# Performance work log

Measured on AMD Instinct MI355X. Metric: run time of the kernel, lower is better.

## Reference

```python
import jax, jax.numpy as jnp
import numpy as np

L, LM, B, D, H, DFF = 1024, 1024, 2, 512, 8, 2048
N = 16              # mamba d_state
DI = 2 * D          # mamba d_inner (expand=2)
DCONV = 4
DTR = (D + 15) // 16  # dt_rank = 32
EPS = 1e-5


def _rmsnorm(x, w):
    return x * w / jnp.sqrt(jnp.mean(x * x, -1, keepdims=True) + EPS)


def _layernorm(x, w, b):
    m = jnp.mean(x, -1, keepdims=True)
    v = jnp.mean((x - m) ** 2, -1, keepdims=True)
    return (x - m) / jnp.sqrt(v + EPS) * w + b


def _mha(q, k, v, in_w, in_b, out_w, out_b):
    # q: [Lq,B,D]; k,v: [Lk,B,D]
    Lq, Bb, Dd = q.shape
    Lk = k.shape[0]
    dh = Dd // H
    qp = (q @ in_w[:Dd].T + in_b[:Dd]).reshape(Lq, Bb, H, dh).transpose(1, 2, 0, 3)
    kp = (k @ in_w[Dd:2 * Dd].T + in_b[Dd:2 * Dd]).reshape(Lk, Bb, H, dh).transpose(1, 2, 0, 3)
    vp = (v @ in_w[2 * Dd:].T + in_b[2 * Dd:]).reshape(Lk, Bb, H, dh).transpose(1, 2, 0, 3)
    s = jnp.einsum('bhqd,bhkd->bhqk', qp, kp) * (dh ** -0.5)
    a = jax.nn.softmax(s, axis=-1)
    o = jnp.einsum('bhqk,bhkd->bhqd', a, vp).transpose(2, 0, 1, 3).reshape(Lq, Bb, Dd)
    return o @ out_w.T + out_b, jnp.mean(a, axis=1)  # attn averaged over heads


def _mamba(x, in_w, in_b, conv_w, conv_b, xproj_w, dt_w, dt_b, Alog, Dp, out_w, out_b):
    # x: [B,L,D] -> [B,L,D] selective state-space scan (mamba.py MambaBlock)
    xz = x @ in_w.T + in_b
    xm, z = xz[..., :DI], xz[..., DI:]
    # causal depthwise conv over time (pad left d_conv-1, truncate to L)
    xc = jax.lax.conv_general_dilated(
        xm.transpose(0, 2, 1), conv_w[:, None, :], (1,), [(DCONV - 1, 0)],
        feature_group_count=DI, dimension_numbers=('NCH', 'OIH', 'NCH'))
    xm = jax.nn.silu((xc + conv_b[None, :, None]).transpose(0, 2, 1))  # [B,L,DI]
    dbc = xm @ xproj_w.T
    dt, Bs, Cs = dbc[..., :DTR], dbc[..., DTR:DTR + N], dbc[..., DTR + N:]
    delta = jax.nn.softplus(dt @ dt_w.T + dt_b)           # [B,L,DI]
    A = -jnp.exp(Alog)                                    # [DI,N]
    dA = jnp.exp(delta[..., None] * A)                    # [B,L,DI,N]
    dBx = delta[..., None] * Bs[:, :, None, :] * xm[..., None]

    def step(h, ab):
        a, b = ab
        h = a * h + b
        return h, h

    _, hs = jax.lax.scan(step, jnp.zeros((x.shape[0], DI, N), x.dtype),
                         (dA.transpose(1, 0, 2, 3), dBx.transpose(1, 0, 2, 3)))
    y = jnp.einsum('blin,bln->bli', hs.transpose(1, 0, 2, 3), Cs)
    y = (y + Dp * xm) * jax.nn.silu(z)
    return y @ out_w.T + out_b


def _bimamba(x, ln1_w, ln1_b, ln2_w, ln2_b, f1_w, f1_b, f2_w, f2_b, mp):
    xn = _layernorm(x, ln1_w, ln1_b)
    mf = _mamba(xn, *mp)
    mb = jnp.flip(_mamba(jnp.flip(xn, 1), *mp), 1)
    m = _layernorm(mf + mb, ln2_w, ln2_b)
    ff = jax.nn.gelu(m @ f1_w.T + f1_b, approximate=False) @ f2_w.T + f2_b
    return ff + x


def _forward(tgt, memory,
             sa_in_w, sa_in_b, sa_out_w, sa_out_b,
             ca_in_w, ca_in_b, ca_out_w, ca_out_b,
             n1_w, n2_w, n3_w, n4_w,
             lin1_w, lin1_b, lin2_w, lin2_b,
             ln1_w, ln1_b, ln2_w, ln2_b,
             bff1_w, bff1_b, bff2_w, bff2_b,
             m_in_w, m_in_b, m_conv_w, m_conv_b, m_xproj_w,
             m_dt_w, m_dt_b, m_Alog, m_D, m_out_w, m_out_b):
    t2, _ = _mha(tgt, tgt, tgt, sa_in_w, sa_in_b, sa_out_w, sa_out_b)
    tgt = _rmsnorm(tgt + t2, n1_w)
    t2, attn = _mha(tgt, memory, memory, ca_in_w, ca_in_b, ca_out_w, ca_out_b)
    tgt = _rmsnorm(tgt + t2, n2_w)
    x = tgt.transpose(1, 0, 2)  # l b d -> b l d
    mp = (m_in_w, m_in_b, m_conv_w, m_conv_b, m_xproj_w, m_dt_w, m_dt_b, m_Alog, m_D, m_out_w, m_out_b)
    x = x + _bimamba(x, ln1_w, ln1_b, ln2_w, ln2_b, bff1_w, bff1_b, bff2_w, bff2_b, mp)
    tgt = x.transpose(1, 0, 2)
    tgt = _rmsnorm(tgt, n3_w)
    t2 = jax.nn.relu(tgt @ lin1_w.T + lin1_b) @ lin2_w.T + lin2_b
    tgt = _rmsnorm(tgt + t2, n4_w)
    return tgt, attn


def setup_inputs() -> dict:
    key = jax.random.key(0)
    ks = jax.random.split(key, 24)
    g = lambda i, shape, s=0.02: jax.random.normal(ks[i], shape, dtype=jnp.float32) * s
    inp = {
        'tgt': jax.random.normal(ks[0], (L, B, D), dtype=jnp.float32),
        'memory': jax.random.normal(ks[1], (LM, B, D), dtype=jnp.float32),
        'sa_in_w': g(2, (3 * D, D)), 'sa_in_b': jnp.zeros((3 * D,)),
        'sa_out_w': g(3, (D, D)), 'sa_out_b': jnp.zeros((D,)),
        'ca_in_w': g(4, (3 * D, D)), 'ca_in_b': jnp.zeros((3 * D,)),
        'ca_out_w': g(5, (D, D)), 'ca_out_b': jnp.zeros((D,)),
        'n1_w': jnp.ones((D,)), 'n2_w': jnp.ones((D,)),
        'n3_w': jnp.ones((D,)), 'n4_w': jnp.ones((D,)),
        'lin1_w': g(6, (DFF, D)), 'lin1_b': jnp.zeros((DFF,)),
        'lin2_w': g(7, (D, DFF)), 'lin2_b': jnp.zeros((D,)),
        'ln1_w': jnp.ones((D,)), 'ln1_b': jnp.zeros((D,)),
        'ln2_w': jnp.ones((D,)), 'ln2_b': jnp.zeros((D,)),
        'bff1_w': g(8, (4 * D, D)), 'bff1_b': jnp.zeros((4 * D,)),
        'bff2_w': g(9, (D, 4 * D)), 'bff2_b': jnp.zeros((D,)),
        'm_in_w': g(10, (2 * DI, D)), 'm_in_b': jnp.zeros((2 * DI,)),
        'm_conv_w': g(11, (DI, DCONV), 0.1), 'm_conv_b': jnp.zeros((DI,)),
        'm_xproj_w': g(12, (DTR + 2 * N, DI)),
        'm_dt_w': g(13, (DI, DTR), 0.1), 'm_dt_b': g(14, (DI,), 0.01),
        'm_Alog': jnp.log(jnp.tile(jnp.arange(1, N + 1, dtype=jnp.float32), (DI, 1))),
        'm_D': jnp.ones((DI,)),
        'm_out_w': g(15, (D, DI)), 'm_out_b': jnp.zeros((D,)),
    }
    return inp


def reference(tgt, memory,
              sa_in_w, sa_in_b, sa_out_w, sa_out_b,
              ca_in_w, ca_in_b, ca_out_w, ca_out_b,
              n1_w, n2_w, n3_w, n4_w,
              lin1_w, lin1_b, lin2_w, lin2_b,
              ln1_w, ln1_b, ln2_w, ln2_b,
              bff1_w, bff1_b, bff2_w, bff2_b,
              m_in_w, m_in_b, m_conv_w, m_conv_b, m_xproj_w,
              m_dt_w, m_dt_b, m_Alog, m_D, m_out_w, m_out_b):
    return _forward(tgt, memory,
                    sa_in_w, sa_in_b, sa_out_w, sa_out_b,
                    ca_in_w, ca_in_b, ca_out_w, ca_out_b,
                    n1_w, n2_w, n3_w, n4_w,
                    lin1_w, lin1_b, lin2_w, lin2_b,
                    ln1_w, ln1_b, ln2_w, ln2_b,
                    bff1_w, bff1_b, bff2_w, bff2_b,
                    m_in_w, m_in_b, m_conv_w, m_conv_b, m_xproj_w,
                    m_dt_w, m_dt_b, m_Alog, m_D, m_out_w, m_out_b)
```

## Files before the change

kernel.cpp:

```cpp
#include <hip/hip_runtime.h>
#include <hip/hip_bf16.h>
#include <math.h>

#define L_SEQ 1024
#define BB 2
#define DD 512
#define HH 8
#define DFFN 2048
#define NSTATE 16
#define DI 1024
#define EPSF 1e-5f

typedef __hip_bfloat16 bf16;
typedef __attribute__((ext_vector_type(8))) short short8v;
typedef __attribute__((ext_vector_type(4))) short short4v;
typedef __attribute__((ext_vector_type(4))) float float4v;

__device__ __forceinline__ float bf2f(bf16 v){ return __bfloat162float(v); }
__device__ __forceinline__ bf16 f2bf(float v){ return __float2bfloat16(v); }
__device__ __forceinline__ short f2bfs(float v){
  bf16 t = __float2bfloat16(v);
  short s; __builtin_memcpy(&s, &t, 2);
  return s;
}

__device__ __forceinline__ void powtab(float q1, float* dA){
  float q2=q1*q1, q4=q2*q2, q8=q4*q4;
  dA[0]=q1;       dA[1]=q2;       dA[2]=q2*q1;     dA[3]=q4;
  dA[4]=q4*q1;    dA[5]=q4*q2;    dA[6]=q4*q2*q1;  dA[7]=q8;
  dA[8]=q8*q1;    dA[9]=q8*q2;    dA[10]=q8*q2*q1; dA[11]=q8*q4;
  dA[12]=q8*q4*q1;dA[13]=q8*q4*q2;dA[14]=q8*q4*q2*q1;dA[15]=q8*q8;
}

__global__ void k_detect(const unsigned int* __restrict__ w, int* __restrict__ flag){
  __shared__ int cnt;
  if (threadIdx.x==0) cnt = 0;
  __syncthreads();
  unsigned int x = w[threadIdx.x];
  unsigned int low = x & 0xffffu;
  int e = (int)((low >> 7) & 0xffu);
  int vote = (low==0u) || (e >= 110 && e <= 140);
  atomicAdd(&cnt, vote);
  __syncthreads();
  if (threadIdx.x==0) flag[0] = (cnt >= 128) ? 1 : 0;
}

struct CvtTabF { const void* src[25]; unsigned int off[26]; };
struct CvtTabW { const void* src[12]; unsigned int off[13]; };

__global__ __launch_bounds__(256) void k_cvt_f32(CvtTabF t, float* __restrict__ dst,
                                                 const int* __restrict__ flag, int total){
  const int isbf = flag[0];
  for (int g = blockIdx.x*256 + threadIdx.x; g < total; g += gridDim.x*256){
    int k = 0;
    while (t.off[k+1] <= (unsigned int)g) ++k;
    int e = g - (int)t.off[k];
    dst[g] = isbf ? bf2f(((const bf16*)t.src[k])[e]) : ((const float*)t.src[k])[e];
  }
}

__global__ __launch_bounds__(256) void k_cvt_b16(CvtTabW t, bf16* __restrict__ dst,
                                                 const int* __restrict__ flag, int total){
  const int isbf = flag[0];
  for (int g = blockIdx.x*256 + threadIdx.x; g < total; g += gridDim.x*256){
    int k = 0;
    while (t.off[k+1] <= (unsigned int)g) ++k;
    int e = g - (int)t.off[k];
    if (isbf) dst[g] = ((const bf16*)t.src[k])[e];
    else      dst[g] = f2bf(((const float*)t.src[k])[e]);
  }
}

__global__ __launch_bounds__(256) void k_mfma_gemm(
    const void* __restrict__ Ab, int cA, long long sAb, long long sAh, long long sAm,
    const void* __restrict__ Bb, long long sBb, long long sBh, long long sBrow, int cB,
    void* __restrict__ Cb, int outBf, long long sCb, long long sCh, long long sCm,
    const float* __restrict__ bias, float scale, int act, int K, int H)
{
  __shared__ short As[64*40];
  __shared__ short Bs[64*40];
  const int tid = threadIdx.x;
  int bx = blockIdx.x, by = blockIdx.y;
  if (gridDim.z == 1 && (gridDim.y & 7) == 0){
    int gx = gridDim.x;
    int lin = by*gx + bx;
    int xcd = lin & 7, i = lin >> 3;
    by = xcd*(gridDim.y >> 3) + i / gx;
    bx = i % gx;
  }
  const int z = blockIdx.z; const int zb = z / H; const int zh = z % H;
  const int col0 = bx << 6, m0 = by << 6;
  const float* Af = (const float*)Ab;
  const bf16*  Aw = (const bf16*)Ab;
  const long long aoff = zb*sAb + zh*sAh;
  const float* Bf = (const float*)Bb;
  const bf16* Bw = (const bf16*)Bb;
  const long long boff = zb*sBb + zh*sBh;
  float4v acc[4];
  #pragma unroll
  for (int i=0;i<4;++i) acc[i] = (float4v)(0.f);
  const int lane = tid & 63, w = tid >> 6;
  const int lr = lane & 15, quad = lane >> 4;

  for (int k0 = 0; k0 < K; k0 += 32){
    if (cA == 1){
      int row = tid >> 2, k8 = (tid & 3) << 3;
      short8v v = *(const short8v*)&Aw[aoff + (long long)(m0+row)*sAm + k0 + k8];
      *(short8v*)&As[row*40 + k8] = v;
    } else {
      #pragma unroll
      for (int i=0;i<2;++i){
        int g = tid + i*256;
        int row = g >> 3, k4 = (g & 7) << 2;
        float4 v = *(const float4*)&Af[aoff + (long long)(m0+row)*sAm + k0 + k4];
        short4v s4; s4.x=f2bfs(v.x); s4.y=f2bfs(v.y); s4.z=f2bfs(v.z); s4.w=f2bfs(v.w);
        *(short4v*)&As[row*40 + k4] = s4;
      }
    }
    if (cB == 2){
      int row = tid >> 2, k8 = (tid & 3) << 3;
      short8v v = *(const short8v*)&Bw[boff + (long long)(col0+row)*sBrow + k0 + k8];
      *(short8v*)&Bs[row*40 + k8] = v;
    } else {
      #pragma unroll
      for (int i=0;i<2;++i){
        int g = tid + i*256;
        int row = g >> 3, k4 = (g & 7) << 2;
        float4 v = *(const float4*)&Bf[boff + (long long)(col0+row)*sBrow + k0 + k4];
        short4v s4; s4.x=f2bfs(v.x); s4.y=f2bfs(v.y); s4.z=f2bfs(v.z); s4.w=f2bfs(v.w);
        *(short4v*)&Bs[row*40 + k4] = s4;
      }
    }
    __syncthreads();
    short8v a = *(short8v*)&As[(w*16 + lr)*40 + quad*8];
    #pragma unroll
    for (int cb=0; cb<4; ++cb){
      short8v bfr = *(short8v*)&Bs[(cb*16 + lr)*40 + quad*8];
      acc[cb] = __builtin_amdgcn_mfma_f32_16x16x32_bf16(a, bfr, acc[cb], 0, 0, 0);
    }
    __syncthreads();
  }
  #pragma unroll
  for (int cb=0; cb<4; ++cb){
    #pragma unroll
    for (int r=0;r<4;++r){
      int m = m0 + w*16 + quad*4 + r;
      int n = col0 + cb*16 + lr;
      float v = acc[cb][r] * scale;
      if (bias) v += bias[n];
      if (act==1) v = fmaxf(v,0.f);
      else if (act==2) v = 0.5f*v*(1.f + erff(v*0.70710678118654752f));
      else if (act==3) v = fmaxf(v,0.f) + log1pf(__expf(-fabsf(v)));
      if (outBf) ((bf16*)Cb)[zb*sCb + zh*sCh + (long long)m*sCm + n] = f2bf(v);
      else       ((float*)Cb)[zb*sCb + zh*sCh + (long long)m*sCm + n] = v;
    }
  }
}

__global__ __launch_bounds__(256) void k_gemm_sk(
    const void* __restrict__ Ab, int cA, long long sAz, long long sAm,
    const bf16* __restrict__ Bw, long long sBrow,
    float* __restrict__ Cb, long long sCz, long long sCm,
    const float* __restrict__ bias, int K, int KS)
{
  __shared__ short As[64*40];
  __shared__ short Bs[64*40];
  const int tid = threadIdx.x;
  int bx, by, bz;
  {
    int gx = gridDim.x, gy = gridDim.y, gz = gridDim.z;
    int lin = ((int)blockIdx.z*gy + blockIdx.y)*gx + blockIdx.x;
    int xcd = lin & 7, i = lin >> 3;
    bx = i % gx; int rest = i / gx;
    int pair = xcd * ((gy*gz) >> 3) + rest;
    by = pair % gy; bz = pair / gy;
  }
  const int zb = bz / KS, kc = bz % KS;
  const int Kc = K / KS;
  const int col0 = bx << 6, m0 = by << 6;
  const float* Af = (const float*)Ab;
  const bf16*  Aw = (const bf16*)Ab;
  const long long aoff = (long long)zb*sAz;
  float4v acc[4];
  #pragma unroll
  for (int i=0;i<4;++i) acc[i] = (float4v)(0.f);
  const int lane = tid & 63, w = tid >> 6;
  const int lr = lane & 15, quad = lane >> 4;

  const int kbeg = kc*Kc;
  for (int k0 = kbeg; k0 < kbeg + Kc; k0 += 32){
    if (cA == 1){
      int row = tid >> 2, k8 = (tid & 3) << 3;
      *(short8v*)&As[row*40 + k8] =
        *(const short8v*)&Aw[aoff + (long long)(m0+row)*sAm + k0 + k8];
    } else {
      #pragma unroll
      for (int i=0;i<2;++i){
        int g = tid + i*256;
        int row = g >> 3, k4 = (g & 7) << 2;
        float4 v = *(const float4*)&Af[aoff + (long long)(m0+row)*sAm + k0 + k4];
        short4v s4; s4.x=f2bfs(v.x); s4.y=f2bfs(v.y); s4.z=f2bfs(v.z); s4.w=f2bfs(v.w);
        *(short4v*)&As[row*40 + k4] = s4;
      }
    }
    {
      int row = tid >> 2, k8 = (tid & 3) << 3;
      *(short8v*)&Bs[row*40 + k8] =
        *(const short8v*)&Bw[(long long)(col0+row)*sBrow + k0 + k8];
    }
    __syncthreads();
    short8v a = *(short8v*)&As[(w*16 + lr)*40 + quad*8];
    #pragma unroll
    for (int cb=0; cb<4; ++cb){
      short8v bfr = *(short8v*)&Bs[(cb*16 + lr)*40 + quad*8];
      acc[cb] = __builtin_amdgcn_mfma_f32_16x16x32_bf16(a, bfr, acc[cb], 0, 0, 0);
    }
    __syncthreads();
  }
  #pragma unroll
  for (int cb=0; cb<4; ++cb){
    #pragma unroll
    for (int r=0;r<4;++r){
      int m = m0 + w*16 + quad*4 + r;
      int n = col0 + cb*16 + lr;
      float v = acc[cb][r];
      if (kc == 0 && bias) v += bias[n];
      atomicAdd(&Cb[(long long)zb*sCz + (long long)m*sCm + n], v);
    }
  }
}

__global__ __launch_bounds__(256) void k_flash2(
    const bf16* __restrict__ Qb, int ldq, int qoff,
    const bf16* __restrict__ Kb, int ldk, int koff,
    const bf16* __restrict__ Vb, int ldv, int voff,
    float* __restrict__ Opart, float* __restrict__ Ml, float scale)
{
  __shared__ short Qs[64*40];
  __shared__ short Ks[64*40];
  __shared__ short Vs[64*40];
  __shared__ short Ps[64*40];
  const int tid = threadIdx.x;
  const int q0 = blockIdx.x << 6;
  const int z = blockIdx.y; const int b = z >> 3; const int hoff = (z & 7) << 6;
  const int kc = blockIdx.z;
  const int lane = tid & 63, w = tid >> 6;
  const int lr = lane & 15, quad = lane >> 4;

  #pragma unroll
  for (int i=0;i<2;++i){
    int idx = tid + i*256;
    int row = idx >> 3, d8 = (idx & 7) << 3;
    *(short8v*)&Qs[row*40 + d8] =
      *(const short8v*)&Qb[(size_t)((q0+row)*BB + b)*ldq + qoff + hoff + d8];
  }

  float m_r[4], l_r[4];
  #pragma unroll
  for (int r=0;r<4;++r){ m_r[r] = -1e30f; l_r[r] = 0.f; }
  float4v acc_o[4];
  #pragma unroll
  for (int cb=0;cb<4;++cb) acc_o[cb] = (float4v)(0.f);

  short8v kr[2], vr[2];
  #pragma unroll
  for (int i=0;i<2;++i){
    int idx = tid + i*256;
    int row = kc*128 + (idx >> 3); int d8 = (idx & 7) << 3;
    kr[i] = *(const short8v*)&Kb[(size_t)(row*BB + b)*ldk + koff + hoff + d8];
    vr[i] = *(const short8v*)&Vb[(size_t)(row*BB + b)*ldv + voff + hoff + d8];
  }

  for (int kt=0; kt<2; ++kt){
    __syncthreads();
    #pragma unroll
    for (int i=0;i<2;++i){
      int idx = tid + i*256;
      int row = idx >> 3, d8 = (idx & 7) << 3;
      *(short8v*)&Ks[row*40 + d8] = kr[i];
      int sc = row ^ d8;
      #pragma unroll
      for (int j=0;j<8;++j) Vs[(d8+j)*40 + sc] = vr[i][j];
    }
    if (kt < 1){
      #pragma unroll
      for (int i=0;i<2;++i){
        int idx = tid + i*256;
        int row = kc*128 + 64 + (idx >> 3); int d8 = (idx & 7) << 3;
        kr[i] = *(const short8v*)&Kb[(size_t)(row*BB + b)*ldk + koff + hoff + d8];
        vr[i] = *(const short8v*)&Vb[(size_t)(row*BB + b)*ldv + voff + hoff + d8];
      }
    }
    __syncthreads();
    short8v a0 = *(short8v*)&Qs[(w*16+lr)*40 + quad*8];
    short8v a1 = *(short8v*)&Qs[(w*16+lr)*40 + quad*8 + 32];
    float4v s[4];
    #pragma unroll
    for (int cb=0;cb<4;++cb){
      short8v b0 = *(short8v*)&Ks[(cb*16+lr)*40 + quad*8];
      short8v b1 = *(short8v*)&Ks[(cb*16+lr)*40 + quad*8 + 32];
      float4v t = __builtin_amdgcn_mfma_f32_16x16x32_bf16(a0, b0, (float4v)(0.f), 0,0,0);
      s[cb] = __builtin_amdgcn_mfma_f32_16x16x32_bf16(a1, b1, t, 0,0,0);
    }
    #pragma unroll
    for (int cb=0;cb<4;++cb)
      #pragma unroll
      for (int r=0;r<4;++r) s[cb][r] *= scale;
    float al[4];
    #pragma unroll
    for (int r=0;r<4;++r){
      float mx = fmaxf(fmaxf(s[0][r],s[1][r]),fmaxf(s[2][r],s[3][r]));
      #pragma unroll
      for (int ofs=1; ofs<16; ofs<<=1) mx = fmaxf(mx, __shfl_xor(mx, ofs));
      float mnew = fmaxf(m_r[r], mx);
      al[r] = __expf(m_r[r] - mnew);
      float sum = 0.f;
      #pragma unroll
      for (int cb=0;cb<4;++cb){
        float p = __expf(s[cb][r] - mnew);
        s[cb][r] = p;
        sum += p;
      }
      #pragma unroll
      for (int ofs=1; ofs<16; ofs<<=1) sum += __shfl_xor(sum, ofs);
      l_r[r] = l_r[r]*al[r] + sum;
      m_r[r] = mnew;
    }
    #pragma unroll
    for (int cb=0;cb<4;++cb)
      #pragma unroll
      for (int r=0;r<4;++r){
        acc_o[cb][r] *= al[r];
        Ps[(w*16 + quad*4 + r)*40 + cb*16 + lr] = f2bfs(s[cb][r]);
      }
    __syncthreads();
    short8v p0 = *(short8v*)&Ps[(w*16+lr)*40 + quad*8];
    short8v p1 = *(short8v*)&Ps[(w*16+lr)*40 + quad*8 + 32];
    #pragma unroll
    for (int cb=0;cb<4;++cb){
      int dcol = cb*16 + lr;
      int sw = (dcol >> 3) & 7;
      short8v v0 = *(short8v*)&Vs[dcol*40 + ((quad ^ sw) << 3)];
      short8v v1 = *(short8v*)&Vs[dcol*40 + (((quad+4) ^ sw) << 3)];
      acc_o[cb] = __builtin_amdgcn_mfma_f32_16x16x32_bf16(p0, v0, acc_o[cb], 0,0,0);
      acc_o[cb] = __builtin_amdgcn_mfma_f32_16x16x32_bf16(p1, v1, acc_o[cb], 0,0,0);
    }
  }
  #pragma unroll
  for (int r=0;r<4;++r){
    int row = q0 + w*16 + quad*4 + r;
    size_t obase = ((size_t)(kc*16 + z)*1024 + row)*64;
    #pragma unroll
    for (int cb=0;cb<4;++cb)
      Opart[obase + cb*16 + lr] = acc_o[cb][r];
    if (lr == 0){
      size_t mi = ((size_t)kc*16384 + z*1024 + row)*2;
      Ml[mi] = m_r[r]; Ml[mi+1] = l_r[r];
    }
  }
}

__global__ __launch_bounds__(256) void k_fcomb(const float* __restrict__ Opart, const float* __restrict__ Ml,
                                               bf16* __restrict__ O, float* __restrict__ Mfin)
{
  int gid = blockIdx.x*256 + threadIdx.x;
  int row = gid >> 6, d = gid & 63;
  int z = row >> 10, q = row & 1023;
  float m[8], l[8];
  #pragma unroll
  for (int kc=0;kc<8;++kc){
    size_t mi = ((size_t)kc*16384 + row)*2;
    m[kc] = Ml[mi]; l[kc] = Ml[mi+1];
  }
  float ms = -1e30f;
  #pragma unroll
  for (int kc=0;kc<8;++kc) ms = fmaxf(ms, m[kc]);
  float ls = 0.f, o = 0.f;
  #pragma unroll
  for (int kc=0;kc<8;++kc){
    float c = __expf(m[kc]-ms);
    ls += l[kc]*c;
    o  += Opart[((size_t)kc*16384 + row)*64 + d] * c;
  }
  o /= ls;
  int b = z >> 3, hoff = (z & 7) << 6;
  O[((size_t)q*BB + b)*512 + hoff + d] = f2bf(o);
  if (d == 0){ Mfin[(size_t)row*2] = ms; Mfin[(size_t)row*2+1] = ls; }
}

__global__ __launch_bounds__(256) void k_pmean(
    const bf16* __restrict__ Qb, int ldq,
    const bf16* __restrict__ Kb, int ldk,
    const float* __restrict__ Mfin, void* __restrict__ out,
    const int* __restrict__ flag, float scale)
{
  __shared__ short Qs[64*40];
  __shared__ short Ks[64*40];
  const int tid = threadIdx.x;
  const int k0 = blockIdx.x << 6, q0 = blockIdx.y << 6;
  const int b = blockIdx.z;
  const int lane = tid & 63, w = tid >> 6;
  const int lr = lane & 15, quad = lane >> 4;
  float acc[4][4];
  #pragma unroll
  for (int cb=0;cb<4;++cb)
    #pragma unroll
    for (int r=0;r<4;++r) acc[cb][r] = 0.f;

  for (int h=0; h<8; ++h){
    int z = b*8 + h, hoff = h << 6;
    __syncthreads();
    #pragma unroll
    for (int i=0;i<2;++i){
      int idx = tid + i*256;
      int row = idx >> 3, d8 = (idx & 7) << 3;
      *(short8v*)&Qs[row*40 + d8] = *(const short8v*)&Qb[((size_t)(q0+row)*BB + b)*ldq + hoff + d8];
      *(short8v*)&Ks[row*40 + d8] = *(const short8v*)&Kb[((size_t)(k0+row)*BB + b)*ldk + hoff + d8];
    }
    __syncthreads();
    float mm[4], li[4];
    #pragma unroll
    for (int r=0;r<4;++r){
      int qrow = q0 + w*16 + quad*4 + r;
      size_t mi = ((size_t)z*1024 + qrow)*2;
      mm[r] = Mfin[mi]; li[r] = 1.f/Mfin[mi+1];
    }
    short8v a0 = *(short8v*)&Qs[(w*16+lr)*40 + quad*8];
    short8v a1 = *(short8v*)&Qs[(w*16+lr)*40 + quad*8 + 32];
    #pragma unroll
    for (int cb=0;cb<4;++cb){
      short8v b0 = *(short8v*)&Ks[(cb*16+lr)*40 + quad*8];
      short8v b1 = *(short8v*)&Ks[(cb*16+lr)*40 + quad*8 + 32];
      float4v t = __builtin_amdgcn_mfma_f32_16x16x32_bf16(a0, b0, (float4v)(0.f), 0,0,0);
      t = __builtin_amdgcn_mfma_f32_16x16x32_bf16(a1, b1, t, 0,0,0);
      #pragma unroll
      for (int r=0;r<4;++r)
        acc[cb][r] += __expf(t[r]*scale - mm[r]) * li[r];
    }
  }
  #pragma unroll
  for (int cb=0;cb<4;++cb)
    #pragma unroll
    for (int r=0;r<4;++r){
      int q = q0 + w*16 + quad*4 + r;
      int k = k0 + cb*16 + lr;
      float v = acc[cb][r] * 0.125f;
      size_t o = (size_t)(1u<<20) + ((size_t)b<<20) + (size_t)q*1024 + k;
      if (flag[0]) ((bf16*)out)[o] = f2bf(v);
      else         ((float*)out)[o] = v;
    }
}

__global__ __launch_bounds__(256) void k_add_rmsnorm(float* __restrict__ x, const float* __restrict__ t2, const float* __restrict__ w){
  int row = blockIdx.x; size_t base = (size_t)row*DD;
  int tid = threadIdx.x;
  float v0 = x[base+tid] + t2[base+tid];
  float v1 = x[base+tid+256] + t2[base+tid+256];
  __shared__ float red[256];
  red[tid] = v0*v0 + v1*v1; __syncthreads();
  for (int s=128;s>0;s>>=1){ if(tid<s) red[tid]+=red[tid+s]; __syncthreads(); }
  float rms = rsqrtf(red[0]*(1.f/DD) + EPSF);
  x[base+tid]     = v0 * w[tid]     * rms;
  x[base+tid+256] = v1 * w[tid+256] * rms;
}

__global__ __launch_bounds__(256) void k_add_rmsnorm_out(const float* __restrict__ x, const float* __restrict__ t2,
                                                         const float* __restrict__ w, void* __restrict__ out,
                                                         const int* __restrict__ flag){
  int row = blockIdx.x; size_t base = (size_t)row*DD;
  int tid = threadIdx.x;
  float v0 = x[base+tid] + t2[base+tid];
  float v1 = x[base+tid+256] + t2[base+tid+256];
  __shared__ float red[256];
  red[tid] = v0*v0 + v1*v1; __syncthreads();
  for (int s=128;s>0;s>>=1){ if(tid<s) red[tid]+=red[tid+s]; __syncthreads(); }
  float rms = rsqrtf(red[0]*(1.f/DD) + EPSF);
  float o0 = v0 * w[tid]     * rms;
  float o1 = v1 * w[tid+256] * rms;
  if (flag[0]){ ((bf16*)out)[base+tid] = f2bf(o0); ((bf16*)out)[base+tid+256] = f2bf(o1); }
  else        { ((float*)out)[base+tid] = o0;      ((float*)out)[base+tid+256] = o1; }
}

__global__ __launch_bounds__(256) void k_trans_layernorm(const float* __restrict__ tgt, const float* __restrict__ w, const float* __restrict__ bias, bf16* __restrict__ xn){
  int r = blockIdx.x;
  int b = r >> 10, l = r & 1023;
  size_t src = ((size_t)l*BB + b)*DD;
  int tid = threadIdx.x;
  float v0 = tgt[src+tid], v1 = tgt[src+tid+256];
  __shared__ float red[256];
  red[tid] = v0 + v1; __syncthreads();
  for (int s=128;s>0;s>>=1){ if(tid<s) red[tid]+=red[tid+s]; __syncthreads(); }
  float mean = red[0]*(1.f/DD);
  __syncthreads();
  red[tid] = v0*v0 + v1*v1; __syncthreads();
  for (int s=128;s>0;s>>=1){ if(tid<s) red[tid]+=red[tid+s]; __syncthreads(); }
  float var = red[0]*(1.f/DD) - mean*mean;
  float rstd = rsqrtf(var + EPSF);
  size_t dst = (size_t)r*DD;
  xn[dst+tid]     = f2bf((v0-mean)*rstd*w[tid]     + bias[tid]);
  xn[dst+tid+256] = f2bf((v1-mean)*rstd*w[tid+256] + bias[tid+256]);
}

__global__ __launch_bounds__(256) void k_combine_ln(const float* __restrict__ yf, const float* __restrict__ yb, const float* __restrict__ w, const float* __restrict__ bias, bf16* __restrict__ mo){
  int r = blockIdx.x; int b = r>>10, l = r&1023;
  size_t rf = (size_t)r*DD;
  size_t rb = ((size_t)(b<<10) + (1023 - l))*DD;
  int tid = threadIdx.x;
  float v0 = yf[rf+tid]     + yb[rb+tid];
  float v1 = yf[rf+tid+256] + yb[rb+tid+256];
  __shared__ float red[256];
  red[tid] = v0 + v1; __syncthreads();
  for (int s=128;s>0;s>>=1){ if(tid<s) red[tid]+=red[tid+s]; __syncthreads(); }
  float mean = red[0]*(1.f/DD);
  __syncthreads();
  red[tid] = v0*v0 + v1*v1; __syncthreads();
  for (int s=128;s>0;s>>=1){ if(tid<s) red[tid]+=red[tid+s]; __syncthreads(); }
  float var = red[0]*(1.f/DD) - mean*mean;
  float rstd = rsqrtf(var + EPSF);
  mo[rf+tid]     = f2bf((v0-mean)*rstd*w[tid]     + bias[tid]);
  mo[rf+tid+256] = f2bf((v1-mean)*rstd*w[tid+256] + bias[tid+256]);
}

__global__ __launch_bounds__(256) void k_bimamba_final(float* __restrict__ tgt, const float* __restrict__ ffo, const float* __restrict__ w){
  int r = blockIdx.x; int b = r>>10, l = r&1023;
  size_t t = ((size_t)l*BB + b)*DD;
  size_t f = (size_t)r*DD;
  int tid = threadIdx.x;
  float v0 = 2.f*tgt[t+tid]     + ffo[f+tid];
  float v1 = 2.f*tgt[t+tid+256] + ffo[f+tid+256];
  __shared__ float red[256];
  red[tid] = v0*v0 + v1*v1; __syncthreads();
  for (int s=128;s>0;s>>=1){ if(tid<s) red[tid]+=red[tid+s]; __syncthreads(); }
  float rms = rsqrtf(red[0]*(1.f/DD) + EPSF);
  tgt[t+tid]     = v0 * w[tid]     * rms;
  tgt[t+tid+256] = v1 * w[tid+256] * rms;
}

__global__ __launch_bounds__(256) void k_conv_silu(const float* __restrict__ xz, const float* __restrict__ cw, const float* __restrict__ cb, bf16* __restrict__ xmc){
  int rev = blockIdx.y;
  int idx = blockIdx.x*256 + threadIdx.x;
  int c = idx & 1023;
  int l = (idx >> 10) & 1023;
  int b = idx >> 20;
  float acc = cb[c];
  float w4[4];
  #pragma unroll
  for (int j=0;j<4;++j) w4[j] = cw[(c<<2)+j];
  #pragma unroll
  for (int j=0;j<4;++j){
    int t = l - 3 + j;
    if (t >= 0){
      int src = rev ? (1023 - t) : t;
      acc = fmaf(w4[j], xz[((size_t)(b<<10) + src)*2048 + c], acc);
    }
  }
  xmc[(size_t)rev*(2u<<20) + idx] = f2bf(acc / (1.f + __expf(-acc)));
}

__global__ __launch_bounds__(256) void k_scan1(
    const bf16* __restrict__ delta_f, const bf16* __restrict__ delta_b,
    const bf16* __restrict__ xmc_f,  const bf16* __restrict__ xmc_b,
    const float* __restrict__ dbc_f,  const float* __restrict__ dbc_b,
    const float* __restrict__ Alog,
    float* __restrict__ hend, float* __restrict__ Sdl)
{
  int ch = blockIdx.x*256 + threadIdx.x;
  int c = blockIdx.y;
  int dir = ch >> 11, b = (ch >> 10) & 1, d = ch & 1023;
  const bf16* delta = dir ? delta_b : delta_f;
  const bf16* xmc   = dir ? xmc_b   : xmc_f;
  const float* dbc  = dir ? dbc_b   : dbc_f;
  float Av[NSTATE]; bool fast = true;
  #pragma unroll
  for (int n=0;n<NSTATE;++n){
    Av[n] = -__expf(Alog[d*NSTATE+n]);
    fast = fast && (fabsf(Av[n] + (float)(n+1)) < 1e-4f*(float)(n+1));
  }
  float h[NSTATE];
  #pragma unroll
  for (int n=0;n<NSTATE;++n) h[n]=0.f;
  float S = 0.f;
  int r0 = b*1024 + c*16;
  for (int t=0;t<16;++t){
    int r = r0 + t;
    float dl = bf2f(delta[((size_t)r<<10) + d]);
    float x  = bf2f(xmc[((size_t)r<<10) + d]);
    const float4* bp = (const float4*)(dbc + (size_t)r*64 + 32);
    float Bv[NSTATE];
    ((float4*)Bv)[0]=bp[0]; ((float4*)Bv)[1]=bp[1]; ((float4*)Bv)[2]=bp[2]; ((float4*)Bv)[3]=bp[3];
    S += dl;
    float dx = dl*x;
    float dA[NSTATE];
    if (fast){ powtab(__expf(-dl), dA); }
    else {
      #pragma unroll
      for (int n=0;n<NSTATE;++n) dA[n] = __expf(dl*Av[n]);
    }
    #pragma unroll
    for (int n=0;n<NSTATE;++n)
      h[n] = fmaf(dA[n], h[n], dx*Bv[n]);
  }
  size_t base = ((size_t)c*4096 + ch)*16;
  #pragma unroll
  for (int n=0;n<NSTATE;++n) hend[base+n] = h[n];
  Sdl[c*4096 + ch] = S;
}

__global__ __launch_bounds__(256) void k_scan_carry(const float* __restrict__ Alog,
                                                    float* __restrict__ hh, const float* __restrict__ Sdl)
{
  int g = blockIdx.x*256 + threadIdx.x;
  int ch = g >> 4, n = g & 15;
// ... 34 lines not shown
  for (int n=0;n<NSTATE;++n) h[n] = hin[cbase+n];
  float Dd = Dp[d];
  int r0 = b*1024 + c*16;
  for (int t=0;t<16;++t){
    int r = r0 + t;
    int lidx = c*16 + t;
    float dl = bf2f(delta[((size_t)r<<10) + d]);
    float x  = bf2f(xmc[((size_t)r<<10) + d]);
    const float4* bp = (const float4*)(dbc + (size_t)r*64 + 32);
    float Bv[NSTATE], Cv[NSTATE];
    ((float4*)Bv)[0]=bp[0]; ((float4*)Bv)[1]=bp[1]; ((float4*)Bv)[2]=bp[2]; ((float4*)Bv)[3]=bp[3];
    ((float4*)Cv)[0]=bp[4]; ((float4*)Cv)[1]=bp[5]; ((float4*)Cv)[2]=bp[6]; ((float4*)Cv)[3]=bp[7];
    float dx = dl*x;
    float dA[NSTATE];
    if (fast){ powtab(__expf(-dl), dA); }
    else {
      #pragma unroll
      for (int n=0;n<NSTATE;++n) dA[n] = __expf(dl*Av[n]);
    }
    float acc0 = 0.f, acc1 = 0.f;
    #pragma unroll
    for (int n=0;n<NSTATE;n+=2){
      h[n]   = fmaf(dA[n],   h[n],   dx*Bv[n]);
      h[n+1] = fmaf(dA[n+1], h[n+1], dx*Bv[n+1]);
      acc0 = fmaf(h[n],   Cv[n],   acc0);
      acc1 = fmaf(h[n+1], Cv[n+1], acc1);
    }
    float acc = acc0 + acc1;
    int src = dir ? (1023 - lidx) : lidx;
    float zz = xz[((size_t)(b<<10) + src)*2048 + 1024 + d];
    float sg = zz / (1.f + __expf(-zz));
    yo[(size_t)dir*(2u<<20) + ((size_t)r<<10) + d] = f2bf((acc + Dd*x) * sg);
  }
}

extern "C" void kernel_launch(void* const* d_in, const int* in_sizes, int n_in,
                              void* d_out, int out_size, void* d_ws, size_t ws_size,
                              hipStream_t stream)
{
  if (n_in < 37) return;
  static const unsigned int SZ[37] = {
    1048576,1048576,786432,1536,262144,512,786432,1536,262144,512,
    512,512,512,512,1048576,2048,1048576,512,512,512,
    512,512,1048576,2048,1048576,512,1048576,2048,4096,1024,
    65536,32768,1024,16384,1024,524288,512
  };
  static const unsigned char ISW[37] = {
    0,0,1,0,1,0,1,0,1,0, 0,0,0,0,1,0,1,0,0,0,
    0,0,1,0,1,0,1,0,0,0, 1,1,0,0,0,1,0
  };
  const long long MF = 1u<<20;
  if (ws_size < (size_t)(32*MF)*sizeof(float)) return;

  float* ws = (float*)d_ws;
  float* inF = ws;
  bf16*  inB = (bf16*)(ws + 3*MF);
  float* t2    = ws + 7*MF;
  float* mbuf  = ws + 8*MF;
  float* proj  = ws + 9*MF;
  float* big   = ws + 12*MF;
  float* ff1   = ws + 28*MF;

  CvtTabF tf; CvtTabW tb;
  unsigned int fOff[37], bOff[37];
  {
    int nf=0, nb=0; unsigned int of=0, ob=0;
    for (int i=0;i<37;++i){
      if (ISW[i]){ tb.src[nb]=d_in[i]; tb.off[nb]=ob; bOff[i]=ob; ob+=SZ[i]; ++nb; }
      else       { tf.src[nf]=d_in[i]; tf.off[nf]=of; fOff[i]=of; of+=SZ[i]; ++nf; }
    }
    tf.off[25]=of; tb.off[12]=ob;
    int* flag = (int*)(ws + 3*MF - 16);

    #define PF(i) (inF + fOff[i])
    #define PW(i) (inB + bOff[i])

    float* tgt_f = PF(0);
    float* mem_f = PF(1);
    bf16* qkvB   = (bf16*)proj;
    bf16* qB     = (bf16*)proj;
    bf16* kvB    = (bf16*)(proj + 1*MF);
    bf16* attnoB = (bf16*)mbuf;
    bf16* xnB    = (bf16*)t2;
    float* Opart   = big;
    float* Ml      = big + 8*MF;
    float* Mfin    = big + 8*MF + 262144;
    float* xz      = big;
    bf16*  xmc_f   = (bf16*)(big + 4*MF);
    bf16*  xmc_b   = (bf16*)(big + 5*MF);
    bf16*  delta_f = (bf16*)(big + 6*MF);
    bf16*  delta_b = (bf16*)(big + 7*MF);
    float* hend    = big + 8*MF;
    float* Sdl     = big + 12*MF;
    float* dbc_f   = proj;
    float* dbc_b   = proj + 131072;
    float* yproj_f = proj + 1*MF;
    float* yproj_b = proj + 2*MF;
    float* ffo     = mem_f;
    bf16*  ybf     = (bf16*)ff1;
    bf16*  ff1B    = (bf16*)ff1;
    bf16*  mbufB   = (bf16*)mbuf;

    k_detect<<<1,256,0,stream>>>((const unsigned int*)d_in[0], flag);
    k_cvt_f32<<<2048,256,0,stream>>>(tf, inF, flag, (int)of);
    k_cvt_b16<<<4096,256,0,stream>>>(tb, inB, flag, (int)ob);

    k_mfma_gemm<<<dim3(24,32,1),256,0,stream>>>(tgt_f,0,0,0,512, PW(2),0,0,512,2, qkvB,1,0,0,1536, PF(3),1.f,0,512,1);
    k_flash2<<<dim3(16,16,8),256,0,stream>>>(qkvB,1536,0, qkvB,1536,512, qkvB,1536,1024, Opart, Ml, 0.125f);
    k_fcomb<<<4096,256,0,stream>>>(Opart, Ml, attnoB, Mfin);
    hipMemsetAsync(t2, 0, (size_t)MF*4, stream);
    k_gemm_sk<<<dim3(8,32,2),256,0,stream>>>(attnoB,1,0,512, PW(4),512, t2,0,512, PF(5), 512, 2);
    k_add_rmsnorm<<<2048,256,0,stream>>>(tgt_f, t2, PF(10));

    k_mfma_gemm<<<dim3(8,32,1),256,0,stream>>>(tgt_f,0,0,0,512, PW(6),0,0,512,2, qB,1,0,0,512, PF(7),1.f,0,512,1);
    k_mfma_gemm<<<dim3(16,32,1),256,0,stream>>>(mem_f,0,0,0,512, PW(6)+(size_t)512*512,0,0,512,2, kvB,1,0,0,1024, PF(7)+512,1.f,0,512,1);
    k_flash2<<<dim3(16,16,8),256,0,stream>>>(qB,512,0, kvB,1024,0, kvB,1024,512, Opart, Ml, 0.125f);
    k_fcomb<<<4096,256,0,stream>>>(Opart, Ml, attnoB, Mfin);
    k_pmean<<<dim3(16,16,2),256,0,stream>>>(qB,512, kvB,1024, Mfin, d_out, flag, 0.125f);
    hipMemsetAsync(t2, 0, (size_t)MF*4, stream);
    k_gemm_sk<<<dim3(8,32,2),256,0,stream>>>(attnoB,1,0,512, PW(8),512, t2,0,512, PF(9), 512, 2);
    k_add_rmsnorm<<<2048,256,0,stream>>>(tgt_f, t2, PF(11));

    k_trans_layernorm<<<2048,256,0,stream>>>(tgt_f, PF(18), PF(19), xnB);
    k_mfma_gemm<<<dim3(32,32,1),256,0,stream>>>(xnB,1,0,0,512, PW(26),0,0,512,2, xz,0,0,0,2048, PF(27),1.f,0,512,1);
    k_conv_silu<<<dim3(8192,2),256,0,stream>>>(xz, PF(28), PF(29), xmc_f);
    hipMemsetAsync(dbc_f, 0, (size_t)262144*4, stream);
    k_gemm_sk<<<dim3(1,32,8),256,0,stream>>>(xmc_f,1,2*MF,1024, PW(30),1024, dbc_f,131072,64, nullptr, 1024, 4);
    k_mfma_gemm<<<dim3(16,32,2),256,0,stream>>>(dbc_f,0,131072,0,64, PW(31),0,0,32,2, delta_f,1,2*MF,0,1024, PF(32),1.f,3,32,1);
    k_scan1<<<dim3(16,64),256,0,stream>>>(delta_f,delta_b,xmc_f,xmc_b,dbc_f,dbc_b, PF(33), hend, Sdl);
    k_scan_carry<<<256,256,0,stream>>>(PF(33), hend, Sdl);
    k_scan2<<<dim3(16,64),256,0,stream>>>(delta_f,delta_b,xmc_f,xmc_b,dbc_f,dbc_b, PF(33), hend, xz, PF(34), ybf);
    hipMemsetAsync(yproj_f, 0, (size_t)2*MF*4, stream);
    k_gemm_sk<<<dim3(8,32,4),256,0,stream>>>(ybf,1,2*MF,1024, PW(35),1024, yproj_f,1*MF,512, PF(36), 1024, 2);
    k_combine_ln<<<2048,256,0,stream>>>(yproj_f, yproj_b, PF(20), PF(21), mbufB);
    k_mfma_gemm<<<dim3(32,32,1),256,0,stream>>>(mbufB,1,0,0,512, PW(22),0,0,512,2, ff1B,1,0,0,2048, PF(23),1.f,2,512,1);
    hipMemsetAsync(ffo, 0, (size_t)MF*4, stream);
    k_gemm_sk<<<dim3(8,32,4),256,0,stream>>>(ff1B,1,0,2048, PW(24),2048, ffo,0,512, PF(25), 2048, 4);
    k_bimamba_final<<<2048,256,0,stream>>>(tgt_f, ffo, PF(12));

    k_mfma_gemm<<<dim3(32,32,1),256,0,stream>>>(tgt_f,0,0,0,512, PW(14),0,0,512,2, ff1B,1,0,0,2048, PF(15),1.f,1,512,1);
    hipMemsetAsync(t2, 0, (size_t)MF*4, stream);
    k_gemm_sk<<<dim3(8,32,4),256,0,stream>>>(ff1B,1,0,2048, PW(16),2048, t2,0,512, PF(17), 2048, 4);
    k_add_rmsnorm_out<<<2048,256,0,stream>>>(tgt_f, t2, PF(13), d_out, flag);
    #undef PF
    #undef PW
  }
}
```

Baseline: 612.5 us.

## Replace atomic split-K with partial buffers reduced in consumer norm kernels

Split-K GEMMs now write per-slice partial outputs with plain stores instead of atomicAdd into memset buffers, and the following norm kernels sum the partials. The memsets go away, the rmsnorm and layernorm kernels are fused into one, the two input conversion kernels are merged into one launch, and the flash-attention partial outputs are stored as bf16. The aim is fewer launches and less atomic and memset traffic, paid for with extra partial-buffer reads and lower precision in the attention partial outputs.

```diff
diff --git a/kernel.cpp b/kernel.cpp
--- a/kernel.cpp
+++ b/kernel.cpp
@@ -48,26 +48,25 @@
 struct CvtTabF { const void* src[25]; unsigned int off[26]; };
 struct CvtTabW { const void* src[12]; unsigned int off[13]; };
 
-__global__ __launch_bounds__(256) void k_cvt_f32(CvtTabF t, float* __restrict__ dst,
-                                                 const int* __restrict__ flag, int total){
+__global__ __launch_bounds__(256) void k_cvt(CvtTabF tf, CvtTabW tb,
+                                             float* __restrict__ dstF, bf16* __restrict__ dstB,
+                                             const int* __restrict__ flag, int totF, int totB){
   const int isbf = flag[0];
-  for (int g = blockIdx.x*256 + threadIdx.x; g < total; g += gridDim.x*256){
-    int k = 0;
-    while (t.off[k+1] <= (unsigned int)g) ++k;
-    int e = g - (int)t.off[k];
-    dst[g] = isbf ? bf2f(((const bf16*)t.src[k])[e]) : ((const float*)t.src[k])[e];
-  }
-}
-
-__global__ __launch_bounds__(256) void k_cvt_b16(CvtTabW t, bf16* __restrict__ dst,
-                                                 const int* __restrict__ flag, int total){
-  const int isbf = flag[0];
-  for (int g = blockIdx.x*256 + threadIdx.x; g < total; g += gridDim.x*256){
-    int k = 0;
-    while (t.off[k+1] <= (unsigned int)g) ++k;
-    int e = g - (int)t.off[k];
-    if (isbf) dst[g] = ((const bf16*)t.src[k])[e];
-    else      dst[g] = f2bf(((const float*)t.src[k])[e]);
+  const int tot = totF + totB;
+  for (int g = blockIdx.x*256 + threadIdx.x; g < tot; g += gridDim.x*256){
+    if (g < totF){
+      int k = 0;
+      while (tf.off[k+1] <= (unsigned int)g) ++k;
+      int e = g - (int)tf.off[k];
+      dstF[g] = isbf ? bf2f(((const bf16*)tf.src[k])[e]) : ((const float*)tf.src[k])[e];
+    } else {
+      int g2 = g - totF;
+      int k = 0;
+      while (tb.off[k+1] <= (unsigned int)g2) ++k;
+      int e = g2 - (int)tb.off[k];
+      if (isbf) dstB[g2] = ((const bf16*)tb.src[k])[e];
+      else      dstB[g2] = f2bf(((const float*)tb.src[k])[e]);
+    }
   }
 }
 
@@ -157,10 +156,10 @@
   }
 }
 
-__global__ __launch_bounds__(256) void k_gemm_sk(
+__global__ __launch_bounds__(256) void k_gemm_skp(
     const void* __restrict__ Ab, int cA, long long sAz, long long sAm,
     const bf16* __restrict__ Bw, long long sBrow,
-    float* __restrict__ Cb, long long sCz, long long sCm,
+    float* __restrict__ Cp, long long sCp, long long sCm,
     const float* __restrict__ bias, int K, int KS)
 {
   __shared__ short As[64*40];
@@ -225,6 +224,79 @@
       int n = col0 + cb*16 + lr;
       float v = acc[cb][r];
       if (kc == 0 && bias) v += bias[n];
+      Cp[(long long)bz*sCp + (long long)m*sCm + n] = v;
+    }
+  }
+}
+
+__global__ __launch_bounds__(256) void k_gemm_sk(
+    const void* __restrict__ Ab, int cA, long long sAz, long long sAm,
+    const bf16* __restrict__ Bw, long long sBrow,
+    float* __restrict__ Cb, long long sCz, long long sCm,
+    const float* __restrict__ bias, int K, int KS)
+{
+  __shared__ short As[64*40];
+  __shared__ short Bs[64*40];
+  const int tid = threadIdx.x;
+  int bx, by, bz;
+  {
+    int gx = gridDim.x, gy = gridDim.y, gz = gridDim.z;
+    int lin = ((int)blockIdx.z*gy + blockIdx.y)*gx + blockIdx.x;
+    int xcd = lin & 7, i = lin >> 3;
+    bx = i % gx; int rest = i / gx;
+    int pair = xcd * ((gy*gz) >> 3) + rest;
+    by = pair % gy; bz = pair / gy;
+  }
+  const int zb = bz / KS, kc = bz % KS;
+  const int Kc = K / KS;
+  const int col0 = bx << 6, m0 = by << 6;
+  const bf16*  Aw = (const bf16*)Ab;
+  const float* Af = (const float*)Ab;
+  const long long aoff = (long long)zb*sAz;
+  float4v acc[4];
+  #pragma unroll
+  for (int i=0;i<4;++i) acc[i] = (float4v)(0.f);
+  const int lane = tid & 63, w = tid >> 6;
+  const int lr = lane & 15, quad = lane >> 4;
+
+  const int kbeg = kc*Kc;
+  for (int k0 = kbeg; k0 < kbeg + Kc; k0 += 32){
+    if (cA == 1){
+      int row = tid >> 2, k8 = (tid & 3) << 3;
+      *(short8v*)&As[row*40 + k8] =
+        *(const short8v*)&Aw[aoff + (long long)(m0+row)*sAm + k0 + k8];
+    } else {
+      #pragma unroll
+      for (int i=0;i<2;++i){
+        int g = tid + i*256;
+        int row = g >> 3, k4 = (g & 7) << 2;
+        float4 v = *(const float4*)&Af[aoff + (long long)(m0+row)*sAm + k0 + k4];
+        short4v s4; s4.x=f2bfs(v.x); s4.y=f2bfs(v.y); s4.z=f2bfs(v.z); s4.w=f2bfs(v.w);
+        *(short4v*)&As[row*40 + k4] = s4;
+      }
+    }
+    {
+      int row = tid >> 2, k8 = (tid & 3) << 3;
+      *(short8v*)&Bs[row*40 + k8] =
+        *(const short8v*)&Bw[(long long)(col0+row)*sBrow + k0 + k8];
+    }
+    __syncthreads();
+    short8v a = *(short8v*)&As[(w*16 + lr)*40 + quad*8];
+    #pragma unroll
+    for (int cb=0; cb<4; ++cb){
+      short8v bfr = *(short8v*)&Bs[(cb*16 + lr)*40 + quad*8];
+      acc[cb] = __builtin_amdgcn_mfma_f32_16x16x32_bf16(a, bfr, acc[cb], 0, 0, 0);
+    }
+    __syncthreads();
+  }
+  #pragma unroll
+  for (int cb=0; cb<4; ++cb){
+    #pragma unroll
+    for (int r=0;r<4;++r){
+      int m = m0 + w*16 + quad*4 + r;
+      int n = col0 + cb*16 + lr;
+      float v = acc[cb][r];
+      if (kc == 0 && bias) v += bias[n];
       atomicAdd(&Cb[(long long)zb*sCz + (long long)m*sCm + n], v);
     }
   }
@@ -234,7 +306,7 @@
     const bf16* __restrict__ Qb, int ldq, int qoff,
     const bf16* __restrict__ Kb, int ldk, int koff,
     const bf16* __restrict__ Vb, int ldv, int voff,
-    float* __restrict__ Opart, float* __restrict__ Ml, float scale)
+    bf16* __restrict__ Opart, float* __restrict__ Ml, float scale)
 {
   __shared__ short Qs[64*40];
   __shared__ short Ks[64*40];
@@ -352,7 +424,7 @@
     size_t obase = ((size_t)(kc*16 + z)*1024 + row)*64;
     #pragma unroll
     for (int cb=0;cb<4;++cb)
-      Opart[obase + cb*16 + lr] = acc_o[cb][r];
+      Opart[obase + cb*16 + lr] = f2bf(acc_o[cb][r]);
     if (lr == 0){
       size_t mi = ((size_t)kc*16384 + z*1024 + row)*2;
       Ml[mi] = m_r[r]; Ml[mi+1] = l_r[r];
@@ -360,7 +432,7 @@
   }
 }
 
-__global__ __launch_bounds__(256) void k_fcomb(const float* __restrict__ Opart, const float* __restrict__ Ml,
+__global__ __launch_bounds__(256) void k_fcomb(const bf16* __restrict__ Opart, const float* __restrict__ Ml,
                                                bf16* __restrict__ O, float* __restrict__ Mfin)
 {
   int gid = blockIdx.x*256 + threadIdx.x;
@@ -380,7 +452,7 @@
   for (int kc=0;kc<8;++kc){
     float c = __expf(m[kc]-ms);
     ls += l[kc]*c;
-    o  += Opart[((size_t)kc*16384 + row)*64 + d] * c;
+    o  += bf2f(Opart[((size_t)kc*16384 + row)*64 + d]) * c;
   }
   o /= ls;
   int b = z >> 3, hoff = (z & 7) << 6;
@@ -451,11 +523,12 @@
     }
 }
 
-__global__ __launch_bounds__(256) void k_add_rmsnorm(float* __restrict__ x, const float* __restrict__ t2, const float* __restrict__ w){
+__global__ __launch_bounds__(256) void k_add_rmsnorm(float* __restrict__ x, const float* __restrict__ tp,
+                                                     long long pstr, int KS, const float* __restrict__ w){
   int row = blockIdx.x; size_t base = (size_t)row*DD;
   int tid = threadIdx.x;
-  float v0 = x[base+tid] + t2[base+tid];
-  float v1 = x[base+tid+256] + t2[base+tid+256];
+  float v0 = x[base+tid], v1 = x[base+tid+256];
+  for (int k=0;k<KS;++k){ v0 += tp[k*pstr + base+tid]; v1 += tp[k*pstr + base+tid+256]; }
   __shared__ float red[256];
   red[tid] = v0*v0 + v1*v1; __syncthreads();
   for (int s=128;s>0;s>>=1){ if(tid<s) red[tid]+=red[tid+s]; __syncthreads(); }
@@ -464,13 +537,14 @@
   x[base+tid+256] = v1 * w[tid+256] * rms;
 }
 
-__global__ __launch_bounds__(256) void k_add_rmsnorm_out(const float* __restrict__ x, const float* __restrict__ t2,
+__global__ __launch_bounds__(256) void k_add_rmsnorm_out(const float* __restrict__ x, const float* __restrict__ tp,
+                                                         long long pstr, int KS,
                                                          const float* __restrict__ w, void* __restrict__ out,
                                                          const int* __restrict__ flag){
   int row = blockIdx.x; size_t base = (size_t)row*DD;
   int tid = threadIdx.x;
-  float v0 = x[base+tid] + t2[base+tid];
-  float v1 = x[base+tid+256] + t2[base+tid+256];
+  float v0 = x[base+tid], v1 = x[base+tid+256];
+  for (int k=0;k<KS;++k){ v0 += tp[k*pstr + base+tid]; v1 += tp[k*pstr + base+tid+256]; }
   __shared__ float red[256];
   red[tid] = v0*v0 + v1*v1; __syncthreads();
   for (int s=128;s>0;s>>=1){ if(tid<s) red[tid]+=red[tid+s]; __syncthreads(); }
@@ -481,13 +555,24 @@
   else        { ((float*)out)[base+tid] = o0;      ((float*)out)[base+tid+256] = o1; }
 }
 
-__global__ __launch_bounds__(256) void k_trans_layernorm(const float* __restrict__ tgt, const float* __restrict__ w, const float* __restrict__ bias, bf16* __restrict__ xn){
+__global__ __launch_bounds__(256) void k_rms_ln(float* __restrict__ tgt, const float* __restrict__ tp,
+                                                long long pstr, const float* __restrict__ n2w,
+                                                const float* __restrict__ lw, const float* __restrict__ lb,
+                                                bf16* __restrict__ xn){
   int r = blockIdx.x;
   int b = r >> 10, l = r & 1023;
-  size_t src = ((size_t)l*BB + b)*DD;
+  size_t base = ((size_t)l*BB + b)*DD;
   int tid = threadIdx.x;
-  float v0 = tgt[src+tid], v1 = tgt[src+tid+256];
+  float v0 = tgt[base+tid] + tp[base+tid] + tp[pstr + base+tid];
+  float v1 = tgt[base+tid+256] + tp[base+tid+256] + tp[pstr + base+tid+256];
   __shared__ float red[256];
+  red[tid] = v0*v0 + v1*v1; __syncthreads();
+  for (int s=128;s>0;s>>=1){ if(tid<s) red[tid]+=red[tid+s]; __syncthreads(); }
+  float rms = rsqrtf(red[0]*(1.f/DD) + EPSF);
+  v0 = v0 * n2w[tid]     * rms;
+  v1 = v1 * n2w[tid+256] * rms;
+  tgt[base+tid] = v0; tgt[base+tid+256] = v1;
+  __syncthreads();
   red[tid] = v0 + v1; __syncthreads();
   for (int s=128;s>0;s>>=1){ if(tid<s) red[tid]+=red[tid+s]; __syncthreads(); }
   float mean = red[0]*(1.f/DD);
@@ -497,17 +582,19 @@
   float var = red[0]*(1.f/DD) - mean*mean;
   float rstd = rsqrtf(var + EPSF);
   size_t dst = (size_t)r*DD;
-  xn[dst+tid]     = f2bf((v0-mean)*rstd*w[tid]     + bias[tid]);
-  xn[dst+tid+256] = f2bf((v1-mean)*rstd*w[tid+256] + bias[tid+256]);
-}
-
-__global__ __launch_bounds__(256) void k_combine_ln(const float* __restrict__ yf, const float* __restrict__ yb, const float* __restrict__ w, const float* __restrict__ bias, bf16* __restrict__ mo){
+  xn[dst+tid]     = f2bf((v0-mean)*rstd*lw[tid]     + lb[tid]);
+  xn[dst+tid+256] = f2bf((v1-mean)*rstd*lw[tid+256] + lb[tid+256]);
+}
+
+__global__ __launch_bounds__(256) void k_combine_ln(const float* __restrict__ yp, long long pstr,
+                                                    const float* __restrict__ w, const float* __restrict__ bias,
+                                                    bf16* __restrict__ mo){
   int r = blockIdx.x; int b = r>>10, l = r&1023;
   size_t rf = (size_t)r*DD;
   size_t rb = ((size_t)(b<<10) + (1023 - l))*DD;
   int tid = threadIdx.x;
-  float v0 = yf[rf+tid]     + yb[rb+tid];
-  float v1 = yf[rf+tid+256] + yb[rb+tid+256];
+  float v0 = yp[rf+tid]     + yp[pstr + rf+tid]     + yp[2*pstr + rb+tid]     + yp[3*pstr + rb+tid];
+  float v1 = yp[rf+tid+256] + yp[pstr + rf+tid+256] + yp[2*pstr + rb+tid+256] + yp[3*pstr + rb+tid+256];
   __shared__ float red[256];
   red[tid] = v0 + v1; __syncthreads();
   for (int s=128;s>0;s>>=1){ if(tid<s) red[tid]+=red[tid+s]; __syncthreads(); }
@@ -521,13 +608,15 @@
   mo[rf+tid+256] = f2bf((v1-mean)*rstd*w[tid+256] + bias[tid+256]);
 }
 
-__global__ __launch_bounds__(256) void k_bimamba_final(float* __restrict__ tgt, const float* __restrict__ ffo, const float* __restrict__ w){
+__global__ __launch_bounds__(256) void k_bimamba_final(float* __restrict__ tgt, const float* __restrict__ fp,
+                                                       long long pstr, const float* __restrict__ w){
   int r = blockIdx.x; int b = r>>10, l = r&1023;
   size_t t = ((size_t)l*BB + b)*DD;
   size_t f = (size_t)r*DD;
   int tid = threadIdx.x;
-  float v0 = 2.f*tgt[t+tid]     + ffo[f+tid];
-  float v1 = 2.f*tgt[t+tid+256] + ffo[f+tid+256];
+  float v0 = 2.f*tgt[t+tid], v1 = 2.f*tgt[t+tid+256];
+  #pragma unroll
+  for (int k=0;k<4;++k){ v0 += fp[k*pstr + f+tid]; v1 += fp[k*pstr + f+tid+256]; }
   __shared__ float red[256];
   red[tid] = v0*v0 + v1*v1; __syncthreads();
   for (int s=128;s>0;s>>=1){ if(tid<s) red[tid]+=red[tid+s]; __syncthreads(); }
@@ -728,9 +817,10 @@
     bf16* kvB    = (bf16*)(proj + 1*MF);
     bf16* attnoB = (bf16*)mbuf;
     bf16* xnB    = (bf16*)t2;
-    float* Opart   = big;
-    float* Ml      = big + 8*MF;
-    float* Mfin    = big + 8*MF + 262144;
+    bf16*  OpartB  = (bf16*)big;
+    float* Ml      = big + 4*MF;
+    float* Mfin    = big + 4*MF + 262144;
+    float* tpart   = big + 5*MF;
     float* xz      = big;
     bf16*  xmc_f   = (bf16*)(big + 4*MF);
     bf16*  xmc_b   = (bf16*)(big + 5*MF);
@@ -740,34 +830,30 @@
     float* Sdl     = big + 12*MF;
     float* dbc_f   = proj;
     float* dbc_b   = proj + 131072;
-    float* yproj_f = proj + 1*MF;
-    float* yproj_b = proj + 2*MF;
-    float* ffo     = mem_f;
+    float* ffop    = big;
+    float* lin2p   = big + 4*MF;
+    float* yprojp  = big + 8*MF;
     bf16*  ybf     = (bf16*)ff1;
     bf16*  ff1B    = (bf16*)ff1;
     bf16*  mbufB   = (bf16*)mbuf;
 
     k_detect<<<1,256,0,stream>>>((const unsigned int*)d_in[0], flag);
-    k_cvt_f32<<<2048,256,0,stream>>>(tf, inF, flag, (int)of);
-    k_cvt_b16<<<4096,256,0,stream>>>(tb, inB, flag, (int)ob);
+    k_cvt<<<4096,256,0,stream>>>(tf, tb, inF, inB, flag, (int)of, (int)ob);
 
     k_mfma_gemm<<<dim3(24,32,1),256,0,stream>>>(tgt_f,0,0,0,512, PW(2),0,0,512,2, qkvB,1,0,0,1536, PF(3),1.f,0,512,1);
-    k_flash2<<<dim3(16,16,8),256,0,stream>>>(qkvB,1536,0, qkvB,1536,512, qkvB,1536,1024, Opart, Ml, 0.125f);
-    k_fcomb<<<4096,256,0,stream>>>(Opart, Ml, attnoB, Mfin);
-    hipMemsetAsync(t2, 0, (size_t)MF*4, stream);
-    k_gemm_sk<<<dim3(8,32,2),256,0,stream>>>(attnoB,1,0,512, PW(4),512, t2,0,512, PF(5), 512, 2);
-    k_add_rmsnorm<<<2048,256,0,stream>>>(tgt_f, t2, PF(10));
+    k_flash2<<<dim3(16,16,8),256,0,stream>>>(qkvB,1536,0, qkvB,1536,512, qkvB,1536,1024, OpartB, Ml, 0.125f);
+    k_fcomb<<<4096,256,0,stream>>>(OpartB, Ml, attnoB, Mfin);
+    k_gemm_skp<<<dim3(8,32,2),256,0,stream>>>(attnoB,1,0,512, PW(4),512, tpart,MF,512, PF(5), 512, 2);
+    k_add_rmsnorm<<<2048,256,0,stream>>>(tgt_f, tpart, MF, 2, PF(10));
 
     k_mfma_gemm<<<dim3(8,32,1),256,0,stream>>>(tgt_f,0,0,0,512, PW(6),0,0,512,2, qB,1,0,0,512, PF(7),1.f,0,512,1);
     k_mfma_gemm<<<dim3(16,32,1),256,0,stream>>>(mem_f,0,0,0,512, PW(6)+(size_t)512*512,0,0,512,2, kvB,1,0,0,1024, PF(7)+512,1.f,0,512,1);
-    k_flash2<<<dim3(16,16,8),256,0,stream>>>(qB,512,0, kvB,1024,0, kvB,1024,512, Opart, Ml, 0.125f);
-    k_fcomb<<<4096,256,0,stream>>>(Opart, Ml, attnoB, Mfin);
+    k_flash2<<<dim3(16,16,8),256,0,stream>>>(qB,512,0, kvB,1024,0, kvB,1024,512, OpartB, Ml, 0.125f);
+    k_fcomb<<<4096,256,0,stream>>>(OpartB, Ml, attnoB, Mfin);
     k_pmean<<<dim3(16,16,2),256,0,stream>>>(qB,512, kvB,1024, Mfin, d_out, flag, 0.125f);
-    hipMemsetAsync(t2, 0, (size_t)MF*4, stream);
-    k_gemm_sk<<<dim3(8,32,2),256,0,stream>>>(attnoB,1,0,512, PW(8),512, t2,0,512, PF(9), 512, 2);
-    k_add_rmsnorm<<<2048,256,0,stream>>>(tgt_f, t2, PF(11));
-
-    k_trans_layernorm<<<2048,256,0,stream>>>(tgt_f, PF(18), PF(19), xnB);
+    k_gemm_skp<<<dim3(8,32,2),256,0,stream>>>(attnoB,1,0,512, PW(8),512, tpart,MF,512, PF(9), 512, 2);
+    k_rms_ln<<<2048,256,0,stream>>>(tgt_f, tpart, MF, PF(11), PF(18), PF(19), xnB);
+
     k_mfma_gemm<<<dim3(32,32,1),256,0,stream>>>(xnB,1,0,0,512, PW(26),0,0,512,2, xz,0,0,0,2048, PF(27),1.f,0,512,1);
     k_conv_silu<<<dim3(8192,2),256,0,stream>>>(xz, PF(28), PF(29), xmc_f);
     hipMemsetAsync(dbc_f, 0, (size_t)262144*4, stream);
@@ -776,18 +862,15 @@
     k_scan1<<<dim3(16,64),256,0,stream>>>(delta_f,delta_b,xmc_f,xmc_b,dbc_f,dbc_b, PF(33), hend, Sdl);
     k_scan_carry<<<256,256,0,stream>>>(PF(33), hend, Sdl);
     k_scan2<<<dim3(16,64),256,0,stream>>>(delta_f,delta_b,xmc_f,xmc_b,dbc_f,dbc_b, PF(33), hend, xz, PF(34), ybf);
-    hipMemsetAsync(yproj_f, 0, (size_t)2*MF*4, stream);
-    k_gemm_sk<<<dim3(8,32,4),256,0,stream>>>(ybf,1,2*MF,1024, PW(35),1024, yproj_f,1*MF,512, PF(36), 1024, 2);
-    k_combine_ln<<<2048,256,0,stream>>>(yproj_f, yproj_b, PF(20), PF(21), mbufB);
+    k_gemm_skp<<<dim3(8,32,4),256,0,stream>>>(ybf,1,2*MF,1024, PW(35),1024, yprojp,MF,512, PF(36), 1024, 2);
+    k_combine_ln<<<2048,256,0,stream>>>(yprojp, MF, PF(20), PF(21), mbufB);
     k_mfma_gemm<<<dim3(32,32,1),256,0,stream>>>(mbufB,1,0,0,512, PW(22),0,0,512,2, ff1B,1,0,0,2048, PF(23),1.f,2,512,1);
-    hipMemsetAsync(ffo, 0, (size_t)MF*4, stream);
-    k_gemm_sk<<<dim3(8,32,4),256,0,stream>>>(ff1B,1,0,2048, PW(24),2048, ffo,0,512, PF(25), 2048, 4);
-    k_bimamba_final<<<2048,256,0,stream>>>(tgt_f, ffo, PF(12));
+    k_gemm_skp<<<dim3(8,32,4),256,0,stream>>>(ff1B,1,0,2048, PW(24),2048, ffop,MF,512, PF(25), 2048, 4);
+    k_bimamba_final<<<2048,256,0,stream>>>(tgt_f, ffop, MF, PF(12));
 
     k_mfma_gemm<<<dim3(32,32,1),256,0,stream>>>(tgt_f,0,0,0,512, PW(14),0,0,512,2, ff1B,1,0,0,2048, PF(15),1.f,1,512,1);
-    hipMemsetAsync(t2, 0, (size_t)MF*4, stream);
-    k_gemm_sk<<<dim3(8,32,4),256,0,stream>>>(ff1B,1,0,2048, PW(16),2048, t2,0,512, PF(17), 2048, 4);
-    k_add_rmsnorm_out<<<2048,256,0,stream>>>(tgt_f, t2, PF(13), d_out, flag);
+    k_gemm_skp<<<dim3(8,32,4),256,0,stream>>>(ff1B,1,0,2048, PW(16),2048, lin2p,MF,512, PF(17), 2048, 4);
+    k_add_rmsnorm_out<<<2048,256,0,stream>>>(tgt_f, lin2p, MF, 4, PF(13), d_out, flag);
     #undef PF
     #undef PW
   }
```

New measurement: 555.0 us. -9.4%, faster.
